# Performance work log

Hardware: AMD Instinct MI355X
Metric: run time of the kernel (lower is better)

The kernel has to match this reference:

```python
import jax, jax.numpy as jnp
import numpy as np


def setup_inputs() -> dict:
    key = jax.random.key(0)
    k1, k2 = jax.random.split(key)
    N = 8192
    means = jax.random.normal(k1, (N, 3), dtype=jnp.float32) * 2.0
    normals = jax.random.normal(k2, (N, 3), dtype=jnp.float32)
    normals = normals / (jnp.linalg.norm(normals, axis=-1, keepdims=True) + 1e-8)
    return {"means": means, "normals": normals, "k": 8}


def reference(means, normals, k):
    # Pairwise Euclidean distances via the ||a-b||^2 expansion: avoids the
    # N x N x 3 diff tensor the original torch code materializes (same math).
    sq = jnp.sum(means * means, axis=-1)                      # (N,)
    d2 = sq[:, None] + sq[None, :] - 2.0 * (means @ means.T)  # (N, N)
    dists = jnp.sqrt(jnp.maximum(d2, 0.0))
    # k+1 smallest distances (self is the 0-distance nearest); drop self.
    dists = jax.lax.stop_gradient(dists)
    _, idx = jax.lax.top_k(-dists, k + 1)                     # (N, k+1)
    idx = idx[:, 1:]                                          # (N, k)
    neighbors = means[idx]                                    # (N, k, 3)
    local_diff = neighbors - means[:, None, :]                # (N, k, 3)
    plane_dist = jnp.sum(local_diff * normals[:, None, :], axis=-1)  # (N, k)
    return jnp.mean(jnp.abs(plane_dist))
```

## Files before the change

kernel.cpp:

```cpp
#include <hip/hip_runtime.h>
#include <hip/hip_bf16.h>

#define NPTS 8192
#define KNN 8
#define RPB 16
#define STAGES 8
#define SCOLS 1024
#define TSEG 8

typedef __attribute__((ext_vector_type(8))) short bf16x8;
typedef __attribute__((ext_vector_type(4))) float f32x4;

__device__ __forceinline__ unsigned int bf16rne(float v) {
    unsigned int u = __float_as_uint(v);
    return (u + 0x7FFFu + ((u >> 16) & 1u)) >> 16;
}
__device__ __forceinline__ float bf2f(unsigned int h) { return __uint_as_float(h << 16); }

__device__ __forceinline__ void insert8(unsigned int (&best)[KNN], unsigned int key) {
#pragma unroll
    for (int t = 0; t < KNN; ++t) {
        const unsigned int lo = min(best[t], key);
        key = max(best[t], key);
        best[t] = lo;
    }
}

__global__ __launch_bounds__(512) void prep_thresh(const float* __restrict__ means,
                                                   float4* __restrict__ pts,
                                                   uint4* __restrict__ cf0,
                                                   uint4* __restrict__ cf1,
                                                   uint4* __restrict__ rf0,
                                                   uint4* __restrict__ rf1,
                                                   float* __restrict__ Tm_arr,
                                                   float* __restrict__ out) {
    __shared__ unsigned int lds_k[TSEG][64][5];
    const int tid = threadIdx.x;
    const int l = tid & 63;
    const int wv = __builtin_amdgcn_readfirstlane(tid >> 6);
    const int pt = blockIdx.x * 64 + l;
    if (blockIdx.x == 0 && tid == 0) out[0] = 0.0f;

    const float x = means[3 * pt + 0];
    const float y = means[3 * pt + 1];
    const float z = means[3 * pt + 2];
    const float sq = x * x + y * y + z * z;
    if (wv == 0) {
        pts[pt] = make_float4(x, y, z, sq);
        const unsigned int hx = bf16rne(x), lx = bf16rne(x - bf2f(hx));
        const unsigned int hy = bf16rne(y), ly = bf16rne(y - bf2f(hy));
        const unsigned int hz = bf16rne(z), lz = bf16rne(z - bf2f(hz));
        const unsigned int hs = bf16rne(sq), ls = bf16rne(sq - bf2f(hs));
        cf0[pt] = make_uint4(hx | (lx << 16), hx | (hy << 16),
                             ly | (hy << 16), hz | (lz << 16));
        cf1[pt] = make_uint4(hz | (hs << 16), ls | (0x3F80u << 16), 0x3F80u, 0u);
        const float ax = -2.0f * x, ay = -2.0f * y, az = -2.0f * z;
        const unsigned int hax = bf16rne(ax), lax = bf16rne(ax - bf2f(hax));
        const unsigned int hay = bf16rne(ay), lay = bf16rne(ay - bf2f(hay));
        const unsigned int haz = bf16rne(az), laz = bf16rne(az - bf2f(haz));
        const unsigned int hsr = bf16rne(sq), lsr = bf16rne(sq - bf2f(hsr));
        rf0[pt] = make_uint4(hax | (hax << 16), lax | (hay << 16),
                             hay | (lay << 16), haz | (haz << 16));
        rf1[pt] = make_uint4(laz | (0x3F80u << 16), 0x3F80u | (hsr << 16), lsr, 0u);
    }

    const float mx2 = -2.0f * x, my2 = -2.0f * y, mz2 = -2.0f * z;
    unsigned int b4[4] = {~0u, ~0u, ~0u, ~0u};
#pragma unroll 4
    for (int m = 0; m < 64; ++m) {
        const int col = 16 * (wv + TSEG * m);
        const float qx = means[3 * col + 0];
        const float qy = means[3 * col + 1];
        const float qz = means[3 * col + 2];
        const float qsq = qx * qx + qy * qy + qz * qz;
        const float d2 = fmaxf(fmaf(mx2, qx, fmaf(my2, qy, fmaf(mz2, qz, sq + qsq))), 0.0f);
        unsigned int key = (__float_as_uint(d2) & 0xFFFFE000u) | (unsigned int)col;
        key = (col == pt) ? ~0u : key;
#pragma unroll
        for (int t = 0; t < 4; ++t) {
            const unsigned int lo = min(b4[t], key);
            key = max(b4[t], key);
            b4[t] = lo;
        }
    }
#pragma unroll
    for (int s = 0; s < 4; ++s) lds_k[wv][l][s] = b4[s];
    __syncthreads();
    if (wv == 0) {
        unsigned int best[KNN] = {b4[0], b4[1], b4[2], b4[3], ~0u, ~0u, ~0u, ~0u};
#pragma unroll
        for (int w = 1; w < TSEG; ++w)
#pragma unroll
            for (int s = 0; s < 4; ++s) insert8(best, lds_k[w][l][s]);
        const float Tf = __uint_as_float(best[7] & 0xFFFFE000u);
        Tm_arr[pt] = Tf + 0.02f + 2e-3f * Tf;
    }
}

__global__ __launch_bounds__(512) void mfma_knn(const uint4* __restrict__ cf0,
                                                const uint4* __restrict__ cf1,
                                                const uint4* __restrict__ rf0,
                                                const uint4* __restrict__ rf1,
                                                const float4* __restrict__ pts,
                                                const float* __restrict__ Tm_arr,
                                                const float* __restrict__ normals,
                                                float* __restrict__ out) {
    __shared__ uint4 lds_cf[2 * SCOLS];
    __shared__ unsigned int km[TSEG][RPB][KNN + 1];
    const int tid = threadIdx.x;
    const int l = tid & 63;
    const int wv = __builtin_amdgcn_readfirstlane(tid >> 6);
    const int R = l & 15;
    const int g = l >> 4;
    const int arow = blockIdx.x * RPB + R;

    const float4 mp = pts[arow];
    const float ax = -2.0f * mp.x, ay = -2.0f * mp.y, az = -2.0f * mp.z;
    const float sq = mp.w;
    const float Tm = Tm_arr[arow];

    uint4 bu = make_uint4(0u, 0u, 0u, 0u);
    if (g == 0) bu = rf0[arow];
    else if (g == 1) bu = rf1[arow];
    union { uint4 u; bf16x8 v; } Bf; Bf.u = bu;
    const f32x4 zero = {0.0f, 0.0f, 0.0f, 0.0f};

    unsigned int best[KNN];
#pragma unroll
    for (int s = 0; s < KNN; ++s) best[s] = ~0u;

    uint4 r0a = cf0[tid], r0b = cf0[512 + tid];
    uint4 r1a = cf1[tid], r1b = cf1[512 + tid];

    for (int s = 0; s < STAGES; ++s) {
        __syncthreads();
        lds_cf[tid] = r0a;            lds_cf[512 + tid] = r0b;
        lds_cf[1024 + tid] = r1a;     lds_cf[1536 + tid] = r1b;
        __syncthreads();
        if (s + 1 < STAGES) {
            const int o = (s + 1) * SCOLS;
            r0a = cf0[o + tid]; r0b = cf0[o + 512 + tid];
            r1a = cf1[o + tid]; r1b = cf1[o + 512 + tid];
        }
        const uint4* __restrict__ asel = (g == 1) ? (lds_cf + SCOLS) : lds_cf;
        unsigned int m = 0u;
#pragma unroll
        for (int mt = 0; mt < 8; ++mt) {
            union { uint4 u; bf16x8 v; } Af;
            Af.u = asel[wv * 128 + mt * 16 + R];
            const f32x4 acc = __builtin_amdgcn_mfma_f32_16x16x32_bf16(Af.v, Bf.v, zero, 0, 0, 0);
#pragma unroll
            for (int r = 0; r < 4; ++r) m = m + m + ((acc[r] <= Tm) ? 1u : 0u);
        }
        while (m) {
            const int b = __ffs(m) - 1;
            m &= m - 1;
            const int t = 31 - b;
            const int col = s * SCOLS + wv * 128 + (t >> 2) * 16 + g * 4 + (t & 3);
            const float4 q = pts[col];
            const float d2 = fmaxf(fmaf(ax, q.x, fmaf(ay, q.y, fmaf(az, q.z, sq + q.w))), 0.0f);
            unsigned int key = (__float_as_uint(d2) & 0xFFFFE000u) | (unsigned int)col;
            key = (col == arow) ? ~0u : key;
            insert8(best, key);
        }
    }

#pragma unroll
    for (int st = 16; st <= 32; st <<= 1) {
        unsigned int tk[KNN];
#pragma unroll
        for (int s = 0; s < KNN; ++s) tk[s] = __shfl_xor(best[s], st);
#pragma unroll
        for (int s = 0; s < KNN; ++s) insert8(best, tk[s]);
    }
    if (l < RPB) {
#pragma unroll
        for (int s = 0; s < KNN; ++s) km[wv][l][s] = best[s];
    }
    for (int st = 1; st < TSEG; st <<= 1) {
        __syncthreads();
        if (((wv & (2 * st - 1)) == 0) && l < RPB) {
#pragma unroll
            for (int s = 0; s < KNN; ++s) insert8(best, km[wv + st][l][s]);
#pragma unroll
            for (int s = 0; s < KNN; ++s) km[wv][l][s] = best[s];
        }
    }

    if (wv == 0) {
        float sum = 0.0f;
        if (l < RPB) {
            const float nx = normals[3 * arow + 0];
            const float ny = normals[3 * arow + 1];
            const float nz = normals[3 * arow + 2];
#pragma unroll
            for (int s = 0; s < KNN; ++s) {
                const int nbr = (int)(best[s] & 0x1FFFu);
                const float4 q = pts[nbr];
                sum += fabsf((q.x - mp.x) * nx + (q.y - mp.y) * ny + (q.z - mp.z) * nz);
            }
        }
#pragma unroll
        for (int off = 8; off > 0; off >>= 1) sum += __shfl_down(sum, off);
        if (l == 0) atomicAdd(out, sum * (1.0f / ((float)NPTS * (float)KNN)));
    }
}

extern "C" void kernel_launch(void* const* d_in, const int* in_sizes, int n_in,
                              void* d_out, int out_size, void* d_ws, size_t ws_size,
                              hipStream_t stream) {
    const float* means = (const float*)d_in[0];
    const float* normals = (const float*)d_in[1];
    float* out = (float*)d_out;
    char* ws = (char*)d_ws;
    uint4* cf0 = (uint4*)ws;
    uint4* cf1 = (uint4*)(ws + 131072);
    uint4* rf0 = (uint4*)(ws + 262144);
    uint4* rf1 = (uint4*)(ws + 393216);
    float4* pts = (float4*)(ws + 524288);
    float* Tm = (float*)(ws + 655360);

    prep_thresh<<<NPTS / 64, 512, 0, stream>>>(means, pts, cf0, cf1, rf0, rf1, Tm, out);
    mfma_knn<<<NPTS / RPB, 512, 0, stream>>>(cf0, cf1, rf0, rf1, pts, Tm, normals, out);
}
```

Measured before the change: 40.69 us.

## Read MFMA column fragments directly from global and parallelize threshold prep

The main kNN kernel stops staging column fragments through LDS with block-wide barriers and register double-buffering. Each wave now loads its A operands straight from global/L2, which removes the two __syncthreads per stage but depends on cache hits for data reuse across blocks. The threshold prep kernel now handles 32 points per block with 16 column classes, and its 8-way sample merge becomes a two-level merge across 128 threads, giving twice as many blocks. Which points are sampled is unchanged.

```diff
diff --git a/kernel.cpp b/kernel.cpp
--- a/kernel.cpp
+++ b/kernel.cpp
@@ -6,7 +6,6 @@
 #define RPB 16
 #define STAGES 8
 #define SCOLS 1024
-#define TSEG 8
 
 typedef __attribute__((ext_vector_type(8))) short bf16x8;
 typedef __attribute__((ext_vector_type(4))) float f32x4;
@@ -23,6 +22,14 @@
         const unsigned int lo = min(best[t], key);
         key = max(best[t], key);
         best[t] = lo;
+    }
+}
+__device__ __forceinline__ void insert4(unsigned int (&b)[4], unsigned int key) {
+#pragma unroll
+    for (int t = 0; t < 4; ++t) {
+        const unsigned int lo = min(b[t], key);
+        key = max(b[t], key);
+        b[t] = lo;
     }
 }
 
@@ -34,18 +41,19 @@
                                                    uint4* __restrict__ rf1,
                                                    float* __restrict__ Tm_arr,
                                                    float* __restrict__ out) {
-    __shared__ unsigned int lds_k[TSEG][64][5];
+    __shared__ unsigned int lds4[16][32][5];
+    __shared__ unsigned int lds8[4][32][8];
     const int tid = threadIdx.x;
-    const int l = tid & 63;
-    const int wv = __builtin_amdgcn_readfirstlane(tid >> 6);
-    const int pt = blockIdx.x * 64 + l;
+    const int pl = tid & 31;
+    const int cls = tid >> 5;
+    const int pt = blockIdx.x * 32 + pl;
     if (blockIdx.x == 0 && tid == 0) out[0] = 0.0f;
 
     const float x = means[3 * pt + 0];
     const float y = means[3 * pt + 1];
     const float z = means[3 * pt + 2];
     const float sq = x * x + y * y + z * z;
-    if (wv == 0) {
+    if (cls == 0) {
         pts[pt] = make_float4(x, y, z, sq);
         const unsigned int hx = bf16rne(x), lx = bf16rne(x - bf2f(hx));
         const unsigned int hy = bf16rne(y), ly = bf16rne(y - bf2f(hy));
@@ -67,8 +75,8 @@
     const float mx2 = -2.0f * x, my2 = -2.0f * y, mz2 = -2.0f * z;
     unsigned int b4[4] = {~0u, ~0u, ~0u, ~0u};
 #pragma unroll 4
-    for (int m = 0; m < 64; ++m) {
-        const int col = 16 * (wv + TSEG * m);
+    for (int m = 0; m < 32; ++m) {
+        const int col = 16 * (cls + 16 * m);
         const float qx = means[3 * col + 0];
         const float qy = means[3 * col + 1];
         const float qz = means[3 * col + 2];
@@ -76,24 +84,32 @@
         const float d2 = fmaxf(fmaf(mx2, qx, fmaf(my2, qy, fmaf(mz2, qz, sq + qsq))), 0.0f);
         unsigned int key = (__float_as_uint(d2) & 0xFFFFE000u) | (unsigned int)col;
         key = (col == pt) ? ~0u : key;
-#pragma unroll
-        for (int t = 0; t < 4; ++t) {
-            const unsigned int lo = min(b4[t], key);
-            key = max(b4[t], key);
-            b4[t] = lo;
-        }
-    }
-#pragma unroll
-    for (int s = 0; s < 4; ++s) lds_k[wv][l][s] = b4[s];
+        insert4(b4, key);
+    }
+#pragma unroll
+    for (int j = 0; j < 4; ++j) lds4[cls][pl][j] = b4[j];
     __syncthreads();
-    if (wv == 0) {
-        unsigned int best[KNN] = {b4[0], b4[1], b4[2], b4[3], ~0u, ~0u, ~0u, ~0u};
-#pragma unroll
-        for (int w = 1; w < TSEG; ++w)
-#pragma unroll
-            for (int s = 0; s < 4; ++s) insert8(best, lds_k[w][l][s]);
-        const float Tf = __uint_as_float(best[7] & 0xFFFFE000u);
-        Tm_arr[pt] = Tf + 0.02f + 2e-3f * Tf;
+    if (tid < 128) {
+        const int p2 = tid & 31, q = tid >> 5;
+        unsigned int bb[KNN];
+#pragma unroll
+        for (int s = 0; s < KNN; ++s) bb[s] = ~0u;
+        for (int c = q * 4; c < q * 4 + 4; ++c)
+#pragma unroll
+            for (int j = 0; j < 4; ++j) insert8(bb, lds4[c][p2][j]);
+#pragma unroll
+        for (int s = 0; s < KNN; ++s) lds8[q][p2][s] = bb[s];
+    }
+    __syncthreads();
+    if (tid < 32) {
+        unsigned int bb[KNN];
+#pragma unroll
+        for (int s = 0; s < KNN; ++s) bb[s] = ~0u;
+        for (int q = 0; q < 4; ++q)
+#pragma unroll
+            for (int s = 0; s < KNN; ++s) insert8(bb, lds8[q][tid][s]);
+        const float Tf = __uint_as_float(bb[7] & 0xFFFFE000u);
+        Tm_arr[blockIdx.x * 32 + tid] = Tf + 0.02f + 2e-3f * Tf;
     }
 }
 
@@ -105,8 +121,7 @@
                                                 const float* __restrict__ Tm_arr,
                                                 const float* __restrict__ normals,
                                                 float* __restrict__ out) {
-    __shared__ uint4 lds_cf[2 * SCOLS];
-    __shared__ unsigned int km[TSEG][RPB][KNN + 1];
+    __shared__ unsigned int km[8][RPB][KNN + 1];
     const int tid = threadIdx.x;
     const int l = tid & 63;
     const int wv = __builtin_amdgcn_readfirstlane(tid >> 6);
@@ -125,29 +140,20 @@
     union { uint4 u; bf16x8 v; } Bf; Bf.u = bu;
     const f32x4 zero = {0.0f, 0.0f, 0.0f, 0.0f};
 
+    const uint4* __restrict__ asel = (g == 1) ? cf1 : cf0;
+
     unsigned int best[KNN];
 #pragma unroll
     for (int s = 0; s < KNN; ++s) best[s] = ~0u;
 
-    uint4 r0a = cf0[tid], r0b = cf0[512 + tid];
-    uint4 r1a = cf1[tid], r1b = cf1[512 + tid];
-
+#pragma unroll 1
     for (int s = 0; s < STAGES; ++s) {
-        __syncthreads();
-        lds_cf[tid] = r0a;            lds_cf[512 + tid] = r0b;
-        lds_cf[1024 + tid] = r1a;     lds_cf[1536 + tid] = r1b;
-        __syncthreads();
-        if (s + 1 < STAGES) {
-            const int o = (s + 1) * SCOLS;
-            r0a = cf0[o + tid]; r0b = cf0[o + 512 + tid];
-            r1a = cf1[o + tid]; r1b = cf1[o + 512 + tid];
-        }
-        const uint4* __restrict__ asel = (g == 1) ? (lds_cf + SCOLS) : lds_cf;
+        const int base = s * SCOLS + wv * 128;
         unsigned int m = 0u;
 #pragma unroll
         for (int mt = 0; mt < 8; ++mt) {
             union { uint4 u; bf16x8 v; } Af;
-            Af.u = asel[wv * 128 + mt * 16 + R];
+            Af.u = asel[base + mt * 16 + R];
             const f32x4 acc = __builtin_amdgcn_mfma_f32_16x16x32_bf16(Af.v, Bf.v, zero, 0, 0, 0);
 #pragma unroll
             for (int r = 0; r < 4; ++r) m = m + m + ((acc[r] <= Tm) ? 1u : 0u);
@@ -156,7 +162,7 @@
             const int b = __ffs(m) - 1;
             m &= m - 1;
             const int t = 31 - b;
-            const int col = s * SCOLS + wv * 128 + (t >> 2) * 16 + g * 4 + (t & 3);
+            const int col = base + (t >> 2) * 16 + g * 4 + (t & 3);
             const float4 q = pts[col];
             const float d2 = fmaxf(fmaf(ax, q.x, fmaf(ay, q.y, fmaf(az, q.z, sq + q.w))), 0.0f);
             unsigned int key = (__float_as_uint(d2) & 0xFFFFE000u) | (unsigned int)col;
@@ -177,7 +183,7 @@
 #pragma unroll
         for (int s = 0; s < KNN; ++s) km[wv][l][s] = best[s];
     }
-    for (int st = 1; st < TSEG; st <<= 1) {
+    for (int st = 1; st < 8; st <<= 1) {
         __syncthreads();
         if (((wv & (2 * st - 1)) == 0) && l < RPB) {
 #pragma unroll
@@ -220,6 +226,6 @@
     float4* pts = (float4*)(ws + 524288);
     float* Tm = (float*)(ws + 655360);
 
-    prep_thresh<<<NPTS / 64, 512, 0, stream>>>(means, pts, cf0, cf1, rf0, rf1, Tm, out);
+    prep_thresh<<<NPTS / 32, 512, 0, stream>>>(means, pts, cf0, cf1, rf0, rf1, Tm, out);
     mfma_knn<<<NPTS / RPB, 512, 0, stream>>>(cf0, cf1, rf0, rf1, pts, Tm, normals, out);
 }
```

After: 35.02 us. 1.16x faster.
